# Kernel tuning notes

Measured on AMD Instinct MI355X. Metric: run time of the kernel, lower is better.

Reference implementation:

```python
import jax, jax.numpy as jnp
import numpy as np

B, L = 4, 2048
D_MODEL, D_STATE, D_CONV, N_BLOCKS = 128, 16, 8, 6
EXPAND = 2
D_INNER = EXPAND * D_MODEL          # 256
DT_RANK = (D_MODEL + 15) // 16      # 8
CONV_K = 7                          # pre_conv kernel


def setup_inputs() -> dict:
    key = jax.random.key(0)
    ks = jax.random.split(key, 10)
    f = lambda k, s: jax.random.normal(k, s, jnp.float32)
    sc = 0.02
    A_init = jnp.broadcast_to(
        jnp.log(jnp.arange(1, D_STATE + 1, dtype=jnp.float32)),
        (N_BLOCKS, D_INNER, D_STATE)) + 0.0
    return {
        "x": f(ks[0], (B, L, 1)),
        "pre_conv_w": f(ks[1], (D_MODEL, 1, CONV_K)) * sc,
        "pre_conv_b": jnp.zeros((D_MODEL,), jnp.float32),
        "ln_w": jnp.ones((N_BLOCKS, D_MODEL), jnp.float32),
        "ln_b": jnp.zeros((N_BLOCKS, D_MODEL), jnp.float32),
        "W_in": f(ks[2], (N_BLOCKS, 2 * D_INNER, D_MODEL)) * sc,
        "conv_w": f(ks[3], (N_BLOCKS, D_INNER, 1, D_CONV)) * sc,  # depthwise OIH
        "conv_b": jnp.zeros((N_BLOCKS, D_INNER), jnp.float32),
        "W_x": f(ks[4], (N_BLOCKS, DT_RANK + 2 * D_STATE, D_INNER)) * sc,
        "W_dt": f(ks[5], (N_BLOCKS, D_INNER, DT_RANK)) * sc,
        "b_dt": jnp.full((N_BLOCKS, D_INNER), -4.6, jnp.float32),  # softplus ~ 0.01
        "A_log": A_init,
        "D_skip": jnp.ones((N_BLOCKS, D_INNER), jnp.float32),
        "W_out": f(ks[6], (N_BLOCKS, D_MODEL, D_INNER)) * sc,
        "out_w": f(ks[7], (1, D_MODEL)) * sc,
        "out_b": jnp.zeros((1,), jnp.float32),
    }


def _layernorm(x, w, b, eps=1e-5):
    m = jnp.mean(x, axis=-1, keepdims=True)
    v = jnp.mean(jnp.square(x - m), axis=-1, keepdims=True)
    return (x - m) * jax.lax.rsqrt(v + eps) * w + b


def _mamba(x, W_in, cw, cb, W_x, W_dt, b_dt, A_log, D_skip, W_out):
    # x: (B, L, D_MODEL)
    xz = jnp.einsum('bld,ed->ble', x, W_in)            # (B,L,2E)
    xi, z = jnp.split(xz, 2, axis=-1)
    # depthwise causal conv over time
    xc = jax.lax.conv_general_dilated(
        xi.transpose(0, 2, 1), cw, window_strides=(1,),
        padding=[(D_CONV - 1, 0)],
        dimension_numbers=('NCH', 'OIH', 'NCH'),
        feature_group_count=D_INNER) + cb[None, :, None]
    xc = jax.nn.silu(xc).transpose(0, 2, 1)            # (B,L,E)
    dbl = jnp.einsum('ble,re->blr', xc, W_x)
    dt = dbl[..., :DT_RANK]
    Bm = dbl[..., DT_RANK:DT_RANK + D_STATE]           # (B,L,N)
    Cm = dbl[..., DT_RANK + D_STATE:]                  # (B,L,N)
    delta = jax.nn.softplus(jnp.einsum('blr,er->ble', dt, W_dt) + b_dt)
    A = -jnp.exp(A_log)                                # (E,N)

    def step(h, inp):
        d, b, c, u = inp                               # (B,E),(B,N),(B,N),(B,E)
        h = h * jnp.exp(d[..., None] * A) + (d * u)[..., None] * b[:, None, :]
        return h, jnp.einsum('ben,bn->be', h, c)

    h0 = jnp.zeros((x.shape[0], D_INNER, D_STATE), x.dtype)
    xs = (delta.transpose(1, 0, 2), Bm.transpose(1, 0, 2),
          Cm.transpose(1, 0, 2), xc.transpose(1, 0, 2))
    _, ys = jax.lax.scan(step, h0, xs)                 # ys: (L,B,E)
    y = ys.transpose(1, 0, 2) + D_skip * xc
    y = y * jax.nn.silu(z)
    return jnp.einsum('ble,de->bld', y, W_out)


def reference(x, pre_conv_w, pre_conv_b, ln_w, ln_b, W_in, conv_w, conv_b,
              W_x, W_dt, b_dt, A_log, D_skip, W_out, out_w, out_b):
    # pre_conv (1 -> d_model), SAME padding, then exact GELU
    h = jax.lax.conv_general_dilated(
        x.transpose(0, 2, 1), pre_conv_w, window_strides=(1,),
        padding=[(CONV_K // 2, CONV_K // 2)],
        dimension_numbers=('NCH', 'OIH', 'NCH')) + pre_conv_b[None, :, None]
    h = jax.nn.gelu(h, approximate=False).transpose(0, 2, 1)  # (B,L,D)

    def block(carry, p):
        lw, lb, Wi, cw, cb, Wx, Wdt, bdt, Alog, Dsk, Wo = p
        y = _mamba(_layernorm(carry, lw, lb), Wi, cw, cb, Wx, Wdt, bdt, Alog, Dsk, Wo)
        return carry + y, None                         # dropout is identity (eval)

    h, _ = jax.lax.scan(block, h, (ln_w, ln_b, W_in, conv_w, conv_b,
                                   W_x, W_dt, b_dt, A_log, D_skip, W_out))
    return (jnp.einsum('bld,od->blo', h, out_w) + out_b)[..., 0]  # (B,L)
```

## Files before the change

### kernel.cpp

```cpp
#include <hip/hip_runtime.h>
#include <hip/hip_bf16.h>
#include <hip/hip_cooperative_groups.h>
#include <math.h>

namespace cg = cooperative_groups;

#define BB 4
#define LL 2048
#define DM 128
#define DI 256
#define DS 16
#define DTR 8
#define NB 6
#define KPRE 7
#define KC 8
#define NC 128
#define CT 16
#define NCHUNK (BB*NC)
#define BL (BB*LL)
#define SU 4

typedef __attribute__((ext_vector_type(8))) short short8v;
typedef __attribute__((ext_vector_type(4))) short short4v;
typedef __attribute__((ext_vector_type(4))) float f32x4;

__device__ __forceinline__ void store_bf16x4(__hip_bfloat16* p, float a, float b, float c, float d) {
    __hip_bfloat16 t[4] = {__float2bfloat16(a), __float2bfloat16(b),
                           __float2bfloat16(c), __float2bfloat16(d)};
    *(short4v*)p = *(const short4v*)t;
}
__device__ __forceinline__ float4 load_bf16x4(const __hip_bfloat16* p) {
    short4v raw = *(const short4v*)p;
    const __hip_bfloat16* t = (const __hip_bfloat16*)&raw;
    return make_float4(__bfloat162float(t[0]), __bfloat162float(t[1]),
                       __bfloat162float(t[2]), __bfloat162float(t[3]));
}


__device__ __forceinline__ void dev_preconv(int idx,
    const float* __restrict__ x, const float* __restrict__ w, const float* __restrict__ bias,
    float* __restrict__ h, const float* __restrict__ Wi, const float* __restrict__ Wo,
    __hip_bfloat16* __restrict__ wi, __hip_bfloat16* __restrict__ wo) {
    int d = idx & (DM - 1);
    int l = (idx >> 7) & (LL - 1);
    int b = idx >> 18;
    float acc = bias[d];
#pragma unroll
    for (int k = 0; k < KPRE; ++k) {
        int pos = l + k - 3;
        float xv = (pos >= 0 && pos < LL) ? x[b * LL + pos] : 0.f;
        acc = fmaf(xv, w[d * KPRE + k], acc);
    }
    h[idx] = 0.5f * acc * (1.f + erff(acc * 0.70710678118654752f));
    if (idx < NB * 2 * DI * DM) wi[idx] = __float2bfloat16(Wi[idx]);
    if (idx < NB * DM * DI)     wo[idx] = __float2bfloat16(Wo[idx]);
}

__device__ __forceinline__ void dev_phaseA(int chunk, int tid,
    const float* __restrict__ h, const float* __restrict__ lw, const float* __restrict__ lb,
    const __hip_bfloat16* __restrict__ Wi,
    const float* __restrict__ cw, const float* __restrict__ cbs,
    const float* __restrict__ Wx, const float* __restrict__ Wdt, const float* __restrict__ bdt,
    const float* __restrict__ A_log,
    __hip_bfloat16* __restrict__ P, __hip_bfloat16* __restrict__ hend,
    __hip_bfloat16* __restrict__ z_bf,
    __hip_bfloat16* As, __hip_bfloat16 (*xi_s)[DI],
    float (*xc_s)[DI], float (*dl_s)[DI], float (*bc_s)[32]) {
    int c = chunk & (NC - 1);
    int b = chunk >> 7;
    int wave = tid >> 6, lane = tid & 63;
    for (int it = 0; it < 8; ++it) {
        int lr = wave * 8 + it;
        int tl = c * CT + lr - 16;
        int sw = (lr & 7) << 3;
        if (tl >= 0) {
            int t = b * LL + tl;
            float v0 = h[t * DM + lane];
            float v1 = h[t * DM + lane + 64];
            float s = v0 + v1;
#pragma unroll
            for (int off = 32; off; off >>= 1) s += __shfl_xor(s, off);
            float mean = s * (1.f / 128.f);
            float d0 = v0 - mean, d1 = v1 - mean;
            float q = d0 * d0 + d1 * d1;
#pragma unroll
            for (int off = 32; off; off >>= 1) q += __shfl_xor(q, off);
            float rstd = rsqrtf(q * (1.f / 128.f) + 1e-5f);
            As[lr * 128 + (lane ^ sw)]        = __float2bfloat16(d0 * rstd * lw[lane] + lb[lane]);
            As[lr * 128 + ((lane + 64) ^ sw)] = __float2bfloat16(d1 * rstd * lw[lane + 64] + lb[lane + 64]);
        } else {
            As[lr * 128 + (lane ^ sw)]        = __float2bfloat16(0.f);
            As[lr * 128 + ((lane + 64) ^ sw)] = __float2bfloat16(0.f);
        }
    }
    __syncthreads();
    {
        int r = lane & 15, kh = lane >> 4;
        short8v af[2][4];
#pragma unroll
        for (int mf = 0; mf < 2; ++mf)
#pragma unroll
            for (int k = 0; k < 4; ++k) {
                int row = mf * 16 + r;
                int cbk = k * 4 + kh;
                af[mf][k] = *(const short8v*)&As[row * 128 + ((cbk ^ (row & 7)) << 3)];
            }
        int nBase = wave * 128;
        for (int nf = 0; nf < 8; ++nf) {
            short8v bfr[4];
#pragma unroll
            for (int k = 0; k < 4; ++k)
                bfr[k] = *(const short8v*)&Wi[(size_t)(nBase + nf * 16 + r) * DM + k * 32 + kh * 8];
            if (wave < 2) {
                f32x4 acc0 = {}, acc1 = {};
#pragma unroll
                for (int k = 0; k < 4; ++k) {
                    acc0 = __builtin_amdgcn_mfma_f32_16x16x32_bf16(af[0][k], bfr[k], acc0, 0, 0, 0);
                    acc1 = __builtin_amdgcn_mfma_f32_16x16x32_bf16(af[1][k], bfr[k], acc1, 0, 0, 0);
                }
#pragma unroll
                for (int rg = 0; rg < 4; ++rg) {
                    xi_s[kh * 4 + rg][nBase + nf * 16 + r]      = __float2bfloat16(acc0[rg]);
                    xi_s[16 + kh * 4 + rg][nBase + nf * 16 + r] = __float2bfloat16(acc1[rg]);
                }
            } else {
                f32x4 acc1 = {};
#pragma unroll
                for (int k = 0; k < 4; ++k)
                    acc1 = __builtin_amdgcn_mfma_f32_16x16x32_bf16(af[1][k], bfr[k], acc1, 0, 0, 0);
#pragma unroll
                for (int rg = 0; rg < 4; ++rg)
                    z_bf[(size_t)(b * LL + c * CT + kh * 4 + rg) * DI
                         + (nBase - 256) + nf * 16 + r] = __float2bfloat16(acc1[rg]);
            }
        }
    }
    __syncthreads();
    for (int i = 0; i < 4; ++i) {
        int lt = wave * 4 + i;
        float xv[4];
        for (int j = 0; j < 4; ++j) {
            int e = lane + 64 * j;
            float4 c0 = *(const float4*)&cw[e * KC];
            float4 c1 = *(const float4*)&cw[e * KC + 4];
            float wts[8] = {c0.x, c0.y, c0.z, c0.w, c1.x, c1.y, c1.z, c1.w};
            float acc = cbs[e];
#pragma unroll
            for (int k = 0; k < KC; ++k)
                acc = fmaf(__bfloat162float(xi_s[lt + 9 + k][e]), wts[k], acc);
            xv[j] = acc / (1.f + __expf(-acc));
            xc_s[lt][e] = xv[j];
        }
        float dt8[8];
        float bcv = 0.f;
#pragma unroll
        for (int o = 0; o < 40; ++o) {
            const float* w = &Wx[o * DI];
            float s = xv[0] * w[lane];
            s = fmaf(xv[1], w[lane + 64], s);
            s = fmaf(xv[2], w[lane + 128], s);
            s = fmaf(xv[3], w[lane + 192], s);
#pragma unroll
            for (int off = 32; off; off >>= 1) s += __shfl_xor(s, off);
            if (o < 8) dt8[o] = s;
            else if (lane == o - 8) bcv = s;
        }
        if (lane < 32) bc_s[lt][lane] = bcv;
        for (int j = 0; j < 4; ++j) {
            int e = lane + 64 * j;
            float s = bdt[e];
#pragma unroll
            for (int r = 0; r < 8; ++r) s = fmaf(dt8[r], Wdt[e * 8 + r], s);
            dl_s[lt][e] = fmaxf(s, 0.f) + log1pf(__expf(-fabsf(s)));
        }
    }
    __syncthreads();
    int e = tid;
    float d16[CT], u16[CT];
#pragma unroll
    for (int l = 0; l < CT; ++l) { d16[l] = dl_s[l][e]; u16[l] = xc_s[l][e]; }
    for (int ng = 0; ng < 4; ++ng) {
        float4 al = *(const float4*)&A_log[e * DS + 4 * ng];
        float Aen[4] = {-__expf(al.x), -__expf(al.y), -__expf(al.z), -__expf(al.w)};
        float hh[4] = {}, Pl[4] = {1.f, 1.f, 1.f, 1.f};
#pragma unroll
        for (int l = 0; l < CT; ++l) {
            float du = d16[l] * u16[l];
            float4 bm = *(const float4*)&bc_s[l][4 * ng];
            float a0 = __expf(d16[l] * Aen[0]);
            float a1 = __expf(d16[l] * Aen[1]);
            float a2 = __expf(d16[l] * Aen[2]);
            float a3 = __expf(d16[l] * Aen[3]);
            hh[0] = fmaf(hh[0], a0, du * bm.x);
            hh[1] = fmaf(hh[1], a1, du * bm.y);
            hh[2] = fmaf(hh[2], a2, du * bm.z);
            hh[3] = fmaf(hh[3], a3, du * bm.w);
            Pl[0] *= a0; Pl[1] *= a1; Pl[2] *= a2; Pl[3] *= a3;
        }
        size_t oidx = (((size_t)(b * NC + c)) * DI + e) * DS + 4 * ng;
        store_bf16x4(&P[oidx], Pl[0], Pl[1], Pl[2], Pl[3]);
        store_bf16x4(&hend[oidx], hh[0], hh[1], hh[2], hh[3]);
    }
}

__device__ __forceinline__ void dev_carry(int gtid,
    const __hip_bfloat16* __restrict__ P, const __hip_bfloat16* __restrict__ hend,
    __hip_bfloat16* __restrict__ hin) {
    int n = gtid & 15;
    int e = (gtid >> 4) & 255;
    int b = gtid >> 12;
    const size_t cs = (size_t)DI * DS;
    size_t idx0 = (((size_t)(b * NC)) * DI + e) * DS + n;
    float carry = 0.f;
    for (int c0 = 0; c0 < NC; c0 += 8) {
        float p[8], he[8];
#pragma unroll
        for (int j = 0; j < 8; ++j) {
            size_t idx = idx0 + (size_t)(c0 + j) * cs;
            p[j]  = __bfloat162float(P[idx]);
            he[j] = __bfloat162float(hend[idx]);
        }
#pragma unroll
        for (int j = 0; j < 8; ++j) {
            hin[idx0 + (size_t)(c0 + j) * cs] = __float2bfloat16(carry);
            carry = fmaf(p[j], carry, he[j]);
        }
    }
}

__device__ __forceinline__ void dev_fusedB(int chunk, int tid,
    const float* __restrict__ A_log, const __hip_bfloat16* __restrict__ hin,
    const __hip_bfloat16* __restrict__ z_bf, const float* __restrict__ Dsk,
    const __hip_bfloat16* __restrict__ Wo, float* __restrict__ hout,
    const float (*xc_s)[DI], const float (*dl_s)[DI], const float (*bc_s)[32],
    __hip_bfloat16 (*y_s)[DI + 8]) {
    int c = chunk & (NC - 1);
    int b = chunk >> 7;
    int base = b * LL + c * CT;
    int e = tid;
    float d16[CT], u16[CT], yacc[CT];
    float dsk = Dsk[e];
#pragma unroll
    for (int l = 0; l < CT; ++l) {
        d16[l] = dl_s[l][e];
        u16[l] = xc_s[l][e];
        yacc[l] = dsk * u16[l];
    }
    for (int ng = 0; ng < 4; ++ng) {
        float4 al = *(const float4*)&A_log[e * DS + 4 * ng];
        float Aen[4] = {-__expf(al.x), -__expf(al.y), -__expf(al.z), -__expf(al.w)};
        float4 h4 = load_bf16x4(&hin[(((size_t)(b * NC + c)) * DI + e) * DS + 4 * ng]);
        float hh[4] = {h4.x, h4.y, h4.z, h4.w};
#pragma unroll
        for (int l = 0; l < CT; ++l) {
            float du = d16[l] * u16[l];
            float4 bm = *(const float4*)&bc_s[l][4 * ng];
            float4 cm = *(const float4*)&bc_s[l][16 + 4 * ng];
            float a0 = __expf(d16[l] * Aen[0]);
            float a1 = __expf(d16[l] * Aen[1]);
            float a2 = __expf(d16[l] * Aen[2]);
            float a3 = __expf(d16[l] * Aen[3]);
            hh[0] = fmaf(hh[0], a0, du * bm.x);
            hh[1] = fmaf(hh[1], a1, du * bm.y);
            hh[2] = fmaf(hh[2], a2, du * bm.z);
            hh[3] = fmaf(hh[3], a3, du * bm.w);
            float p = hh[0] * cm.x;
            p = fmaf(hh[1], cm.y, p);
            p = fmaf(hh[2], cm.z, p);
            p = fmaf(hh[3], cm.w, p);
            yacc[l] += p;
        }
    }
#pragma unroll
    for (int l = 0; l < CT; ++l) {
        float z = __bfloat162float(z_bf[(size_t)(base + l) * DI + e]);
        y_s[l][e] = __float2bfloat16(yacc[l] * (z / (1.f + __expf(-z))));
    }
    __syncthreads();
    int wave = tid >> 6, lane = tid & 63;
    int r  = lane & 15;
    int kh = lane >> 4;
    f32x4 acc[2] = {};
    for (int k0 = 0; k0 < DI; k0 += 32) {
        short8v af = *(const short8v*)&y_s[r][k0 + kh * 8];
        short8v bf[2];
#pragma unroll
        for (int j = 0; j < 2; ++j)
            bf[j] = *(const short8v*)&Wo[(size_t)(wave * 32 + j * 16 + r) * DI + k0 + kh * 8];
#pragma unroll
        for (int j = 0; j < 2; ++j)
            acc[j] = __builtin_amdgcn_mfma_f32_16x16x32_bf16(af, bf[j], acc[j], 0, 0, 0);
    }
    __syncthreads();
#pragma unroll
    for (int j = 0; j < 2; ++j)
#pragma unroll
        for (int rg = 0; rg < 4; ++rg) {
            size_t off = (size_t)(base + kh * 4 + rg) * DM + wave * 32 + j * 16 + r;
            hout[off] += acc[j][rg];
        }
}

__device__ __forceinline__ void dev_out(int t, int lane,
    const float* __restrict__ h, const float* __restrict__ ow, const float* __restrict__ ob,
    float* __restrict__ out) {
    float s = h[t * DM + lane] * ow[lane] + h[t * DM + lane + 64] * ow[lane + 64];
#pragma unroll
    for (int off = 32; off; off >>= 1) s += __shfl_xor(s, off);
    if (lane == 0) out[t] = s + ob[0];
}


__device__ __forceinline__ void dev_ln_gemm1(int v, int wave, int lane,
    const float* __restrict__ h, const float* __restrict__ lw, const float* __restrict__ lb,
    const __hip_bfloat16* __restrict__ W, float* __restrict__ xz,
    __hip_bfloat16* As) {
    int tileM = v >> 2, tileN = v & 3;
    int mBase = tileM * 64, nBase = tileN * 128;
    for (int it = 0; it < 16; ++it) {
        int row = wave * 16 + it;
        int t = mBase + row;
        float v0 = h[t * DM + lane];
        float v1 = h[t * DM + lane + 64];
        float s = v0 + v1;
#pragma unroll
        for (int off = 32; off; off >>= 1) s += __shfl_xor(s, off);
        float mean = s * (1.f / 128.f);
        float d0 = v0 - mean, d1 = v1 - mean;
        float q = d0 * d0 + d1 * d1;
#pragma unroll
        for (int off = 32; off; off >>= 1) q += __shfl_xor(q, off);
        float rstd = rsqrtf(q * (1.f / 128.f) + 1e-5f);
        int sw = (row & 7) << 3;
        As[row * 128 + (lane ^ sw)]        = __float2bfloat16(d0 * rstd * lw[lane] + lb[lane]);
        As[row * 128 + ((lane + 64) ^ sw)] = __float2bfloat16(d1 * rstd * lw[lane + 64] + lb[lane + 64]);
    }
    __syncthreads();
    int r  = lane & 15;
    int kh = lane >> 4;
    f32x4 acc[4][2] = {};
    for (int k0 = 0; k0 < DM; k0 += 32) {
        short8v af[4], bf[2];
#pragma unroll
        for (int i = 0; i < 4; ++i) {
            int row = i * 16 + r;
            int cbk = (k0 >> 3) + kh;
            af[i] = *(const short8v*)&As[row * 128 + ((cbk ^ (row & 7)) << 3)];
        }
#pragma unroll
        for (int j = 0; j < 2; ++j)
            bf[j] = *(const short8v*)&W[(size_t)(nBase + wave * 32 + j * 16 + r) * DM + k0 + kh * 8];
#pragma unroll
        for (int i = 0; i < 4; ++i)
#pragma unroll
            for (int j = 0; j < 2; ++j)
                acc[i][j] = __builtin_amdgcn_mfma_f32_16x16x32_bf16(af[i], bf[j], acc[i][j], 0, 0, 0);
    }
#pragma unroll
    for (int i = 0; i < 4; ++i)
#pragma unroll
        for (int j = 0; j < 2; ++j)
#pragma unroll
            for (int rg = 0; rg < 4; ++rg) {
                size_t off = (size_t)(mBase + i * 16 + kh * 4 + rg) * (2 * DI)
                           + nBase + wave * 32 + j * 16 + r;
                xz[off] = acc[i][j][rg];
            }
    __syncthreads();
}

__device__ __forceinline__ void dev_conv_wx(int t, int lane,
    const float* __restrict__ xz, const float* __restrict__ cw, const float* __restrict__ cbs,
    const float* __restrict__ Wx, const float* __restrict__ Wdt, const float* __restrict__ bdt,
    float* __restrict__ xc, float* __restrict__ BC, float* __restrict__ delta) {
    int tl = t & (LL - 1);
    int b = t >> 11;
    float xv[4];
#pragma unroll
    for (int j = 0; j < 4; ++j) {
        int e = lane + 64 * j;
        float4 cw0 = *(const float4*)&cw[e * KC];
        float4 cw1 = *(const float4*)&cw[e * KC + 4];
        float wts[8] = {cw0.x, cw0.y, cw0.z, cw0.w, cw1.x, cw1.y, cw1.z, cw1.w};
        float acc = cbs[e];
#pragma unroll
        for (int k = 0; k < KC; ++k) {
            int pos = tl + k - (KC - 1);
            float v = (pos >= 0) ? xz[((size_t)(b * LL + pos) << 9) + e] : 0.f;
            acc = fmaf(v, wts[k], acc);
        }
        xv[j] = acc / (1.f + __expf(-acc));
        xc[((size_t)t << 8) + e] = xv[j];
    }
    float dt[8];
    float bcv = 0.f;
#pragma unroll
    for (int o = 0; o < 40; ++o) {
        const float* w = &Wx[o * DI];
        float s = xv[0] * w[lane];
        s = fmaf(xv[1], w[lane + 64], s);
        s = fmaf(xv[2], w[lane + 128], s);
        s = fmaf(xv[3], w[lane + 192], s);
#pragma unroll
        for (int off = 32; off; off >>= 1) s += __shfl_xor(s, off);
        if (o < 8) dt[o] = s;
        else if (lane == o - 8) bcv = s;
    }
    if (lane < 32) BC[((size_t)t << 5) + lane] = bcv;
#pragma unroll
    for (int j = 0; j < 4; ++j) {
        int e = lane + 64 * j;
        float s = bdt[e];
#pragma unroll
        for (int r = 0; r < 8; ++r) s = fmaf(dt[r], Wdt[e * 8 + r], s);
        delta[((size_t)t << 8) + e] = fmaxf(s, 0.f) + log1pf(__expf(-fabsf(s)));
    }
}

__device__ __forceinline__ void dev_scan1(int blk, int tid,
    const float* __restrict__ delta, const float* __restrict__ xc, const float* __restrict__ BC,
    const float* __restrict__ A_log,
    __hip_bfloat16* __restrict__ P, __hip_bfloat16* __restrict__ hend) {
    int eg = blk & 3;
    int c = (blk >> 2) & (NC - 1);
    int b = blk >> 9;
    int e = eg * 64 + (tid >> 2);
    int ng = tid & 3;
    float4 al = *(const float4*)&A_log[e * DS + 4 * ng];
    float Aen[4] = {-__expf(al.x), -__expf(al.y), -__expf(al.z), -__expf(al.w)};
    float h[4] = {}, Pl[4] = {1.f, 1.f, 1.f, 1.f};
    int base = b * LL + c * CT;
    const float* dp = delta + (size_t)base * DI + e;
    const float* up = xc + (size_t)base * DI + e;
    const float* bp = BC + (size_t)base * 32 + 4 * ng;
    for (int l0 = 0; l0 < CT; l0 += SU) {
        float d[SU], u[SU];
        float4 bm[SU];
#pragma unroll
        for (int j = 0; j < SU; ++j) {
            d[j]  = dp[(l0 + j) * DI];
            u[j]  = up[(l0 + j) * DI];
            bm[j] = *(const float4*)&bp[(l0 + j) * 32];
        }
#pragma unroll
        for (int j = 0; j < SU; ++j) {
            float du = d[j] * u[j];
            float a0 = __expf(d[j] * Aen[0]);
            float a1 = __expf(d[j] * Aen[1]);
            float a2 = __expf(d[j] * Aen[2]);
            float a3 = __expf(d[j] * Aen[3]);
            h[0] = fmaf(h[0], a0, du * bm[j].x);
            h[1] = fmaf(h[1], a1, du * bm[j].y);
            h[2] = fmaf(h[2], a2, du * bm[j].z);
            h[3] = fmaf(h[3], a3, du * bm[j].w);
            Pl[0] *= a0; Pl[1] *= a1; Pl[2] *= a2; Pl[3] *= a3;
        }
    }
    size_t oidx = (((size_t)(b * NC + c)) * DI + e) * DS + 4 * ng;
    store_bf16x4(&P[oidx], Pl[0], Pl[1], Pl[2], Pl[3]);
    store_bf16x4(&hend[oidx], h[0], h[1], h[2], h[3]);
}

__device__ __forceinline__ void dev_scan3(int blk, int tid,
    const float* __restrict__ delta, const float* __restrict__ xc, const float* __restrict__ BC,
    const float* __restrict__ A_log, const __hip_bfloat16* __restrict__ hin,
    const float* __restrict__ xz,
    const float* __restrict__ Dsk, __hip_bfloat16* __restrict__ y) {
    int eg = blk & 3;
    int c = (blk >> 2) & (NC - 1);
    int b = blk >> 9;
    int e = eg * 64 + (tid >> 2);
    int ng = tid & 3;
    float4 al = *(const float4*)&A_log[e * DS + 4 * ng];
    float Aen[4] = {-__expf(al.x), -__expf(al.y), -__expf(al.z), -__expf(al.w)};
    float dsk = Dsk[e];
    float4 h4 = load_bf16x4(&hin[(((size_t)(b * NC + c)) * DI + e) * DS + 4 * ng]);
    float h[4] = {h4.x, h4.y, h4.z, h4.w};
    int base = b * LL + c * CT;
    const float* dp = delta + (size_t)base * DI + e;
    const float* up = xc + (size_t)base * DI + e;
    const float* bp = BC + (size_t)base * 32 + 4 * ng;
    const float* zp = xz + ((size_t)base << 9) + DI + e;
    __hip_bfloat16* yp = y + (size_t)base * DI + e;
    for (int l0 = 0; l0 < CT; l0 += SU) {
        float d[SU], u[SU], zv[SU];
        float4 bm[SU], cm[SU];
#pragma unroll
        for (int j = 0; j < SU; ++j) {
            d[j]  = dp[(l0 + j) * DI];
            u[j]  = up[(l0 + j) * DI];
            bm[j] = *(const float4*)&bp[(l0 + j) * 32];
            cm[j] = *(const float4*)&bp[(l0 + j) * 32 + 16];
            zv[j] = zp[(size_t)(l0 + j) << 9];
        }
#pragma unroll
        for (int j = 0; j < SU; ++j) {
            float du = d[j] * u[j];
            float a0 = __expf(d[j] * Aen[0]);
            float a1 = __expf(d[j] * Aen[1]);
            float a2 = __expf(d[j] * Aen[2]);
            float a3 = __expf(d[j] * Aen[3]);
            h[0] = fmaf(h[0], a0, du * bm[j].x);
            h[1] = fmaf(h[1], a1, du * bm[j].y);
            h[2] = fmaf(h[2], a2, du * bm[j].z);
            h[3] = fmaf(h[3], a3, du * bm[j].w);
            float yc = h[0] * cm[j].x;
            yc = fmaf(h[1], cm[j].y, yc);
            yc = fmaf(h[2], cm[j].z, yc);
            yc = fmaf(h[3], cm[j].w, yc);
            yc += __shfl_xor(yc, 1);
            yc += __shfl_xor(yc, 2);
            if (ng == 0) {
                float z = zv[j];
                float val = (yc + dsk * u[j]) * (z / (1.f + __expf(-z)));
                yp[(l0 + j) * DI] = __float2bfloat16(val);
            }
        }
    }
}

__device__ __forceinline__ void dev_gemm2(int v, int wave, int lane,
    const __hip_bfloat16* __restrict__ A, const __hip_bfloat16* __restrict__ W,
    float* __restrict__ C) {
    int mBase = v * 16;
    int r  = lane & 15;
    int kh = lane >> 4;
    f32x4 acc[2] = {};
    for (int k0 = 0; k0 < DI; k0 += 32) {
        short8v af = *(const short8v*)&A[(size_t)(mBase + r) * DI + k0 + kh * 8];
        short8v bf[2];
#pragma unroll
        for (int j = 0; j < 2; ++j)
            bf[j] = *(const short8v*)&W[(size_t)(wave * 32 + j * 16 + r) * DI + k0 + kh * 8];
#pragma unroll
        for (int j = 0; j < 2; ++j)
            acc[j] = __builtin_amdgcn_mfma_f32_16x16x32_bf16(af, bf[j], acc[j], 0, 0, 0);
    }
#pragma unroll
    for (int j = 0; j < 2; ++j)
#pragma unroll
        for (int rg = 0; rg < 4; ++rg) {
            size_t off = (size_t)(mBase + kh * 4 + rg) * DM + wave * 32 + j * 16 + r;
            C[off] += acc[j][rg];
        }
}


struct MegaArgs {
    const float *x, *pcw, *pcb, *ln_w, *ln_b, *conv_w, *conv_b;
    const float *W_x, *W_dt, *b_dt, *A_log, *D_skip, *W_in, *W_out, *out_w, *out_b;
    float *h, *out;
    __hip_bfloat16 *P, *hend, *hin, *z_bf, *wi_bf, *wo_bf;
};

__global__ __launch_bounds__(256, 2) void k_mega(MegaArgs a) {
    __shared__ union {
        struct {
            __hip_bfloat16 As[32 * 128];
            __hip_bfloat16 xi[32][DI];
        } pa;
        __hip_bfloat16 y_s[CT][DI + 8];
    } u;
    __shared__ float xc_s[CT][DI];
    __shared__ float dl_s[CT][DI];
    __shared__ float bc_s[CT][32];
    cg::grid_group g = cg::this_grid();
    int bid = blockIdx.x, tid = threadIdx.x;
    int nb = gridDim.x;
    int wave = tid >> 6, lane = tid & 63;

    for (int v = bid; v < (BB * LL * DM) / 256; v += nb)
        dev_preconv(v * 256 + tid, a.x, a.pcw, a.pcb, a.h, a.W_in, a.W_out, a.wi_bf, a.wo_bf);
    g.sync();

    for (int blk = 0; blk < NB; ++blk) {
        dev_phaseA(bid, tid, a.h, a.ln_w + blk * DM, a.ln_b + blk * DM,
                   a.wi_bf + (size_t)blk * 2 * DI * DM,
                   a.conv_w + (size_t)blk * DI * KC, a.conv_b + blk * DI,
                   a.W_x + (size_t)blk * 40 * DI, a.W_dt + (size_t)blk * DI * DTR,
                   a.b_dt + blk * DI, a.A_log + (size_t)blk * DI * DS,
                   a.P, a.hend, a.z_bf, u.pa.As, u.pa.xi, xc_s, dl_s, bc_s);
        g.sync();
        for (int v = bid; v < (BB * DI * DS) / 256; v += nb)
            dev_carry(v * 256 + tid, a.P, a.hend, a.hin);
        g.sync();
        dev_fusedB(bid, tid, a.A_log + (size_t)blk * DI * DS, a.hin, a.z_bf,
                   a.D_skip + blk * DI, a.wo_bf + (size_t)blk * DM * DI, a.h,
                   xc_s, dl_s, bc_s, u.y_s);
        g.sync();
    }

    for (int v = bid; v < BL / 4; v += nb)
        dev_out(v * 4 + wave, lane, a.h, a.out_w, a.out_b, a.out);
}


__global__ void w_preconv(const float* x, const float* w, const float* bias, float* h,
                          const float* Wi, const float* Wo,
                          __hip_bfloat16* wi, __hip_bfloat16* wo) {
    dev_preconv(blockIdx.x * 256 + threadIdx.x, x, w, bias, h, Wi, Wo, wi, wo);
}
__global__ __launch_bounds__(256) void w_ln_gemm1(const float* h, const float* lw, const float* lb,
                                                  const __hip_bfloat16* W, float* xz) {
    __shared__ __hip_bfloat16 As[64 * 128];
    dev_ln_gemm1(blockIdx.x, threadIdx.x >> 6, threadIdx.x & 63, h, lw, lb, W, xz, As);
}
__global__ __launch_bounds__(256) void w_conv_wx(const float* xz, const float* cw, const float* cbs,
                                                 const float* Wx, const float* Wdt, const float* bdt,
                                                 float* xc, float* BC, float* delta) {
    dev_conv_wx(blockIdx.x * 4 + (threadIdx.x >> 6), threadIdx.x & 63,
                xz, cw, cbs, Wx, Wdt, bdt, xc, BC, delta);
}
__global__ __launch_bounds__(256) void w_scan1(const float* delta, const float* xc, const float* BC,
                                               const float* A_log,
                                               __hip_bfloat16* P, __hip_bfloat16* hend) {
    dev_scan1(blockIdx.x, threadIdx.x, delta, xc, BC, A_log, P, hend);
}
__global__ void w_carry(const __hip_bfloat16* P, const __hip_bfloat16* hend, __hip_bfloat16* hin) {
    dev_carry(blockIdx.x * 256 + threadIdx.x, P, hend, hin);
}
__global__ __launch_bounds__(256) void w_scan3(const float* delta, const float* xc, const float* BC,
                                               const float* A_log, const __hip_bfloat16* hin,
                                               const float* xz,
                                               const float* Dsk, __hip_bfloat16* y) {
    dev_scan3(blockIdx.x, threadIdx.x, delta, xc, BC, A_log, hin, xz, Dsk, y);
}
__global__ __launch_bounds__(256) void w_gemm2(const __hip_bfloat16* A, const __hip_bfloat16* W,
                                               float* C) {
    dev_gemm2(blockIdx.x, threadIdx.x >> 6, threadIdx.x & 63, A, W, C);
}
__global__ void w_out(const float* h, const float* ow, const float* ob, float* out) {
    dev_out(blockIdx.x * 4 + (threadIdx.x >> 6), threadIdx.x & 63, h, ow, ob, out);
}

extern "C" void kernel_launch(void* const* d_in, const int* in_sizes, int n_in,
                              void* d_out, int out_size, void* d_ws, size_t ws_size,
                              hipStream_t stream) {
    (void)in_sizes; (void)n_in; (void)out_size; (void)ws_size;
    const float* x      = (const float*)d_in[0];
    const float* pcw    = (const float*)d_in[1];
    const float* pcb    = (const float*)d_in[2];
    const float* ln_w   = (const float*)d_in[3];
    const float* ln_b   = (const float*)d_in[4];
    const float* W_in   = (const float*)d_in[5];
    const float* conv_w = (const float*)d_in[6];
    const float* conv_b = (const float*)d_in[7];
    const float* W_x    = (const float*)d_in[8];
    const float* W_dt   = (const float*)d_in[9];
    const float* b_dt   = (const float*)d_in[10];
    const float* A_log  = (const float*)d_in[11];
    const float* D_skip = (const float*)d_in[12];
    const float* W_out  = (const float*)d_in[13];
    const float* out_w  = (const float*)d_in[14];
    const float* out_b  = (const float*)d_in[15];

    const size_t SCAN_N = (size_t)BB * NC * DI * DS;
    float* ws    = (float*)d_ws;
    float* h     = ws;
    float* xz    = h     + (size_t)BL * DM;
    float* xc    = xz    + (size_t)BL * 2 * DI;
    float* BC    = xc    + (size_t)BL * DI;
    float* delta = BC    + (size_t)BL * 2 * DS;
    __hip_bfloat16* P    = (__hip_bfloat16*)(delta + (size_t)BL * DI);
    __hip_bfloat16* hend = P + SCAN_N;
    __hip_bfloat16* hin  = hend + SCAN_N;
    __hip_bfloat16* y_bf  = hin + SCAN_N;
    __hip_bfloat16* z_bf  = y_bf + (size_t)BL * DI;
    __hip_bfloat16* wi_bf = z_bf + (size_t)BL * DI;
    __hip_bfloat16* wo_bf = wi_bf + (size_t)NB * 2 * DI * DM;

    int dev = 0;
    (void)hipGetDevice(&dev);
    int coopAttr = 0;
    (void)hipDeviceGetAttribute(&coopAttr, hipDeviceAttributeCooperativeLaunch, dev);
    int numCU = 0;
    (void)hipDeviceGetAttribute(&numCU, hipDeviceAttributeMultiprocessorCount, dev);
    int maxBpCU = 0;
    (void)hipOccupancyMaxActiveBlocksPerMultiprocessor(&maxBpCU, k_mega, 256, 0);
    int grid = maxBpCU * numCU;
    if (grid > NCHUNK) grid = NCHUNK;

    bool launched = false;
    if (coopAttr && grid == NCHUNK) {
        MegaArgs ma = {x, pcw, pcb, ln_w, ln_b, conv_w, conv_b,
                       W_x, W_dt, b_dt, A_log, D_skip, W_in, W_out, out_w, out_b,
                       h, (float*)d_out,
                       P, hend, hin, z_bf, wi_bf, wo_bf};
        void* kp[] = {&ma};
        hipError_t e = hipLaunchCooperativeKernel((void*)k_mega, dim3(grid), dim3(256), kp, 0, stream);
        launched = (e == hipSuccess);
        if (!launched) (void)hipGetLastError();
    }

    if (!launched) {
        w_preconv<<<(BB * LL * DM) / 256, 256, 0, stream>>>(x, pcw, pcb, h, W_in, W_out, wi_bf, wo_bf);
        for (int blk = 0; blk < NB; ++blk) {
            w_ln_gemm1<<<512, 256, 0, stream>>>(
                h, ln_w + blk * DM, ln_b + blk * DM, wi_bf + (size_t)blk * 2 * DI * DM, xz);
            w_conv_wx<<<BL / 4, 256, 0, stream>>>(
                xz, conv_w + (size_t)blk * DI * KC, conv_b + blk * DI,
                W_x + (size_t)blk * 40 * DI, W_dt + (size_t)blk * DI * DTR,
                b_dt + blk * DI, xc, BC, delta);
            w_scan1<<<BB * NC * 4, 256, 0, stream>>>(
                delta, xc, BC, A_log + (size_t)blk * DI * DS, P, hend);
            w_carry<<<(BB * DI * DS) / 256, 256, 0, stream>>>(P, hend, hin);
            w_scan3<<<BB * NC * 4, 256, 0, stream>>>(
                delta, xc, BC, A_log + (size_t)blk * DI * DS, hin, xz, D_skip + blk * DI, y_bf);
            w_gemm2<<<BL / 16, 256, 0, stream>>>(y_bf, wo_bf + (size_t)blk * DM * DI, h);
        }
        w_out<<<BL / 4, 256, 0, stream>>>(h, out_w, out_b, (float*)d_out);
    }
}
```

Baseline: 562.0 us.

## Replace grid-wide carry pass with decoupled look-back chunk scan and LDS-resident z

Removes the two grid syncs and the separate carry phase in each block. Each chunk now publishes its aggregate (P, hend) and inclusive state through per-chunk flags, then walks back over its predecessors until it finds an inclusive prefix, in the style of a decoupled look-back scan. The z half of the input projection and the chunk's incoming state now stay in shared memory instead of making a round trip through global buffers. This adds spin-waiting on flags with serial dependencies across chunks, and raises LDS use, which may reduce occupancy.

```diff
diff --git a/kernel.cpp b/kernel.cpp
--- a/kernel.cpp
+++ b/kernel.cpp
@@ -35,6 +35,21 @@
     return make_float4(__bfloat162float(t[0]), __bfloat162float(t[1]),
                        __bfloat162float(t[2]), __bfloat162float(t[3]));
 }
+__device__ __forceinline__ void load_bf16x16(const __hip_bfloat16* p, float* o) {
+    short8v a = *(const short8v*)p;
+    short8v b = *(const short8v*)(p + 8);
+    const __hip_bfloat16* ta = (const __hip_bfloat16*)&a;
+    const __hip_bfloat16* tb = (const __hip_bfloat16*)&b;
+#pragma unroll
+    for (int i = 0; i < 8; ++i) { o[i] = __bfloat162float(ta[i]); o[8 + i] = __bfloat162float(tb[i]); }
+}
+__device__ __forceinline__ void store_bf16x16(__hip_bfloat16* p, const float* v) {
+    __hip_bfloat16 t[16];
+#pragma unroll
+    for (int i = 0; i < 16; ++i) t[i] = __float2bfloat16(v[i]);
+    *(short8v*)p = *(const short8v*)t;
+    *(short8v*)(p + 8) = *(const short8v*)(t + 8);
+}
 
 
 __device__ __forceinline__ void dev_preconv(int idx,
@@ -56,16 +71,17 @@
     if (idx < NB * DM * DI)     wo[idx] = __float2bfloat16(Wo[idx]);
 }
 
-__device__ __forceinline__ void dev_phaseA(int chunk, int tid,
+__device__ __forceinline__ void dev_phaseA(int chunk, int tid, int epoch,
     const float* __restrict__ h, const float* __restrict__ lw, const float* __restrict__ lb,
     const __hip_bfloat16* __restrict__ Wi,
     const float* __restrict__ cw, const float* __restrict__ cbs,
     const float* __restrict__ Wx, const float* __restrict__ Wdt, const float* __restrict__ bdt,
     const float* __restrict__ A_log,
-    __hip_bfloat16* __restrict__ P, __hip_bfloat16* __restrict__ hend,
-    __hip_bfloat16* __restrict__ z_bf,
+    __hip_bfloat16* __restrict__ Pst, __hip_bfloat16* __restrict__ hend,
+    __hip_bfloat16* __restrict__ hincl, int* __restrict__ flags,
     __hip_bfloat16* As, __hip_bfloat16 (*xi_s)[DI],
-    float (*xc_s)[DI], float (*dl_s)[DI], float (*bc_s)[32]) {
+    float (*xc_s)[DI], float (*dl_s)[DI], float (*bc_s)[32],
+    __hip_bfloat16 (*z_s)[DI], __hip_bfloat16 (*hin_s)[DS]) {
     int c = chunk & (NC - 1);
     int b = chunk >> 7;
     int wave = tid >> 6, lane = tid & 63;
@@ -130,8 +146,7 @@
                     acc1 = __builtin_amdgcn_mfma_f32_16x16x32_bf16(af[1][k], bfr[k], acc1, 0, 0, 0);
 #pragma unroll
                 for (int rg = 0; rg < 4; ++rg)
-                    z_bf[(size_t)(b * LL + c * CT + kh * 4 + rg) * DI
-                         + (nBase - 256) + nf * 16 + r] = __float2bfloat16(acc1[rg]);
+                    z_s[kh * 4 + rg][(nBase - 256) + nf * 16 + r] = __float2bfloat16(acc1[rg]);
             }
         }
     }
@@ -176,63 +191,101 @@
     }
     __syncthreads();
     int e = tid;
-    float d16[CT], u16[CT];
-#pragma unroll
-    for (int l = 0; l < CT; ++l) { d16[l] = dl_s[l][e]; u16[l] = xc_s[l][e]; }
-    for (int ng = 0; ng < 4; ++ng) {
-        float4 al = *(const float4*)&A_log[e * DS + 4 * ng];
-        float Aen[4] = {-__expf(al.x), -__expf(al.y), -__expf(al.z), -__expf(al.w)};
-        float hh[4] = {}, Pl[4] = {1.f, 1.f, 1.f, 1.f};
-#pragma unroll
-        for (int l = 0; l < CT; ++l) {
-            float du = d16[l] * u16[l];
-            float4 bm = *(const float4*)&bc_s[l][4 * ng];
-            float a0 = __expf(d16[l] * Aen[0]);
-            float a1 = __expf(d16[l] * Aen[1]);
-            float a2 = __expf(d16[l] * Aen[2]);
-            float a3 = __expf(d16[l] * Aen[3]);
-            hh[0] = fmaf(hh[0], a0, du * bm.x);
-            hh[1] = fmaf(hh[1], a1, du * bm.y);
-            hh[2] = fmaf(hh[2], a2, du * bm.z);
-            hh[3] = fmaf(hh[3], a3, du * bm.w);
-            Pl[0] *= a0; Pl[1] *= a1; Pl[2] *= a2; Pl[3] *= a3;
-        }
-        size_t oidx = (((size_t)(b * NC + c)) * DI + e) * DS + 4 * ng;
-        store_bf16x4(&P[oidx], Pl[0], Pl[1], Pl[2], Pl[3]);
-        store_bf16x4(&hend[oidx], hh[0], hh[1], hh[2], hh[3]);
-    }
-}
-
-__device__ __forceinline__ void dev_carry(int gtid,
-    const __hip_bfloat16* __restrict__ P, const __hip_bfloat16* __restrict__ hend,
-    __hip_bfloat16* __restrict__ hin) {
-    int n = gtid & 15;
-    int e = (gtid >> 4) & 255;
-    int b = gtid >> 12;
-    const size_t cs = (size_t)DI * DS;
-    size_t idx0 = (((size_t)(b * NC)) * DI + e) * DS + n;
-    float carry = 0.f;
-    for (int c0 = 0; c0 < NC; c0 += 8) {
-        float p[8], he[8];
-#pragma unroll
-        for (int j = 0; j < 8; ++j) {
-            size_t idx = idx0 + (size_t)(c0 + j) * cs;
-            p[j]  = __bfloat162float(P[idx]);
-            he[j] = __bfloat162float(hend[idx]);
-        }
-#pragma unroll
-        for (int j = 0; j < 8; ++j) {
-            hin[idx0 + (size_t)(c0 + j) * cs] = __float2bfloat16(carry);
-            carry = fmaf(p[j], carry, he[j]);
-        }
-    }
+    {
+        float d16[CT], u16[CT];
+#pragma unroll
+        for (int l = 0; l < CT; ++l) { d16[l] = dl_s[l][e]; u16[l] = xc_s[l][e]; }
+        for (int ng = 0; ng < 4; ++ng) {
+            float4 al = *(const float4*)&A_log[e * DS + 4 * ng];
+            float Aen[4] = {-__expf(al.x), -__expf(al.y), -__expf(al.z), -__expf(al.w)};
+            float hh[4] = {}, Pl[4] = {1.f, 1.f, 1.f, 1.f};
+#pragma unroll
+            for (int l = 0; l < CT; ++l) {
+                float du = d16[l] * u16[l];
+                float4 bm = *(const float4*)&bc_s[l][4 * ng];
+                float a0 = __expf(d16[l] * Aen[0]);
+                float a1 = __expf(d16[l] * Aen[1]);
+                float a2 = __expf(d16[l] * Aen[2]);
+                float a3 = __expf(d16[l] * Aen[3]);
+                hh[0] = fmaf(hh[0], a0, du * bm.x);
+                hh[1] = fmaf(hh[1], a1, du * bm.y);
+                hh[2] = fmaf(hh[2], a2, du * bm.z);
+                hh[3] = fmaf(hh[3], a3, du * bm.w);
+                Pl[0] *= a0; Pl[1] *= a1; Pl[2] *= a2; Pl[3] *= a3;
+            }
+            size_t oidx = (((size_t)(b * NC + c)) * DI + e) * DS + 4 * ng;
+            store_bf16x4(&Pst[oidx], Pl[0], Pl[1], Pl[2], Pl[3]);
+            store_bf16x4(&hend[oidx], hh[0], hh[1], hh[2], hh[3]);
+        }
+    }
+    __threadfence();
+    __syncthreads();
+    if (tid == 0)
+        __hip_atomic_store(&flags[b * NC + c], 2 * epoch,
+                           __ATOMIC_RELEASE, __HIP_MEMORY_SCOPE_AGENT);
+    float hacc[16], Pacc[16];
+#pragma unroll
+    for (int n = 0; n < 16; ++n) { hacc[n] = 0.f; Pacc[n] = 1.f; }
+    int j = c - 1;
+    while (j >= 0) {
+        int j2 = (j >= 1) ? j - 1 : j;
+        int f1, f0;
+        do {
+            f1 = __hip_atomic_load(&flags[b * NC + j],  __ATOMIC_ACQUIRE, __HIP_MEMORY_SCOPE_AGENT);
+            f0 = __hip_atomic_load(&flags[b * NC + j2], __ATOMIC_ACQUIRE, __HIP_MEMORY_SCOPE_AGENT);
+            if (f1 < 2 * epoch || f0 < 2 * epoch) __builtin_amdgcn_s_sleep(2);
+        } while (f1 < 2 * epoch || f0 < 2 * epoch);
+        size_t bj = (((size_t)(b * NC + j)) * DI + e) * DS;
+        if (f1 > 2 * epoch) {
+            float hi[16]; load_bf16x16(&hincl[bj], hi);
+#pragma unroll
+            for (int n = 0; n < 16; ++n) hacc[n] = fmaf(Pacc[n], hi[n], hacc[n]);
+            break;
+        }
+        float pj[16], he[16];
+        load_bf16x16(&Pst[bj], pj);
+        load_bf16x16(&hend[bj], he);
+#pragma unroll
+        for (int n = 0; n < 16; ++n) { hacc[n] = fmaf(Pacc[n], he[n], hacc[n]); Pacc[n] *= pj[n]; }
+        if (j == 0) break;
+        size_t bj0 = (((size_t)(b * NC + j - 1)) * DI + e) * DS;
+        if (f0 > 2 * epoch) {
+            float hi[16]; load_bf16x16(&hincl[bj0], hi);
+#pragma unroll
+            for (int n = 0; n < 16; ++n) hacc[n] = fmaf(Pacc[n], hi[n], hacc[n]);
+            break;
+        }
+        float pj0[16], he0[16];
+        load_bf16x16(&Pst[bj0], pj0);
+        load_bf16x16(&hend[bj0], he0);
+#pragma unroll
+        for (int n = 0; n < 16; ++n) { hacc[n] = fmaf(Pacc[n], he0[n], hacc[n]); Pacc[n] *= pj0[n]; }
+        j -= 2;
+    }
+    {
+        size_t bcx = (((size_t)(b * NC + c)) * DI + e) * DS;
+        float pc[16], hc[16];
+        load_bf16x16(&Pst[bcx], pc);
+        load_bf16x16(&hend[bcx], hc);
+#pragma unroll
+        for (int n = 0; n < 16; ++n) {
+            hin_s[e][n] = __float2bfloat16(hacc[n]);
+            hc[n] = fmaf(pc[n], hacc[n], hc[n]);
+        }
+        store_bf16x16(&hincl[bcx], hc);
+    }
+    __threadfence();
+    __syncthreads();
+    if (tid == 0)
+        __hip_atomic_store(&flags[b * NC + c], 2 * epoch + 1,
+                           __ATOMIC_RELEASE, __HIP_MEMORY_SCOPE_AGENT);
 }
 
 __device__ __forceinline__ void dev_fusedB(int chunk, int tid,
-    const float* __restrict__ A_log, const __hip_bfloat16* __restrict__ hin,
-    const __hip_bfloat16* __restrict__ z_bf, const float* __restrict__ Dsk,
+    const float* __restrict__ A_log, const float* __restrict__ Dsk,
     const __hip_bfloat16* __restrict__ Wo, float* __restrict__ hout,
     const float (*xc_s)[DI], const float (*dl_s)[DI], const float (*bc_s)[32],
+    const __hip_bfloat16 (*z_s)[DI], const __hip_bfloat16 (*hin_s)[DS],
     __hip_bfloat16 (*y_s)[DI + 8]) {
     int c = chunk & (NC - 1);
     int b = chunk >> 7;
@@ -249,8 +302,10 @@
     for (int ng = 0; ng < 4; ++ng) {
         float4 al = *(const float4*)&A_log[e * DS + 4 * ng];
         float Aen[4] = {-__expf(al.x), -__expf(al.y), -__expf(al.z), -__expf(al.w)};
-        float4 h4 = load_bf16x4(&hin[(((size_t)(b * NC + c)) * DI + e) * DS + 4 * ng]);
-        float hh[4] = {h4.x, h4.y, h4.z, h4.w};
+        float hh[4] = {__bfloat162float(hin_s[e][4 * ng]),
+                       __bfloat162float(hin_s[e][4 * ng + 1]),
+                       __bfloat162float(hin_s[e][4 * ng + 2]),
+                       __bfloat162float(hin_s[e][4 * ng + 3])};
 #pragma unroll
         for (int l = 0; l < CT; ++l) {
             float du = d16[l] * u16[l];
@@ -273,7 +328,7 @@
     }
 #pragma unroll
     for (int l = 0; l < CT; ++l) {
-        float z = __bfloat162float(z_bf[(size_t)(base + l) * DI + e]);
+        float z = __bfloat162float(z_s[l][e]);
         y_s[l][e] = __float2bfloat16(yacc[l] * (z / (1.f + __expf(-z))));
     }
     __syncthreads();
@@ -285,19 +340,19 @@
         short8v af = *(const short8v*)&y_s[r][k0 + kh * 8];
         short8v bf[2];
 #pragma unroll
-        for (int j = 0; j < 2; ++j)
-            bf[j] = *(const short8v*)&Wo[(size_t)(wave * 32 + j * 16 + r) * DI + k0 + kh * 8];
-#pragma unroll
-        for (int j = 0; j < 2; ++j)
-            acc[j] = __builtin_amdgcn_mfma_f32_16x16x32_bf16(af, bf[j], acc[j], 0, 0, 0);
-    }
-    __syncthreads();
-#pragma unroll
-    for (int j = 0; j < 2; ++j)
+        for (int jj = 0; jj < 2; ++jj)
+            bf[jj] = *(const short8v*)&Wo[(size_t)(wave * 32 + jj * 16 + r) * DI + k0 + kh * 8];
+#pragma unroll
+        for (int jj = 0; jj < 2; ++jj)
+            acc[jj] = __builtin_amdgcn_mfma_f32_16x16x32_bf16(af, bf[jj], acc[jj], 0, 0, 0);
+    }
+    __syncthreads();
+#pragma unroll
+    for (int jj = 0; jj < 2; ++jj)
 #pragma unroll
         for (int rg = 0; rg < 4; ++rg) {
-            size_t off = (size_t)(base + kh * 4 + rg) * DM + wave * 32 + j * 16 + r;
-            hout[off] += acc[j][rg];
+            size_t off = (size_t)(base + kh * 4 + rg) * DM + wave * 32 + jj * 16 + r;
+            hout[off] += acc[jj][rg];
         }
 }
 
@@ -459,6 +514,31 @@
     size_t oidx = (((size_t)(b * NC + c)) * DI + e) * DS + 4 * ng;
     store_bf16x4(&P[oidx], Pl[0], Pl[1], Pl[2], Pl[3]);
     store_bf16x4(&hend[oidx], h[0], h[1], h[2], h[3]);
+}
+
+__device__ __forceinline__ void dev_carry(int gtid,
+    const __hip_bfloat16* __restrict__ P, const __hip_bfloat16* __restrict__ hend,
+    __hip_bfloat16* __restrict__ hin) {
+    int n = gtid & 15;
+    int e = (gtid >> 4) & 255;
+    int b = gtid >> 12;
+    const size_t cs = (size_t)DI * DS;
+    size_t idx0 = (((size_t)(b * NC)) * DI + e) * DS + n;
+    float carry = 0.f;
+    for (int c0 = 0; c0 < NC; c0 += 8) {
+        float p[8], he[8];
+#pragma unroll
+        for (int j = 0; j < 8; ++j) {
+            size_t idx = idx0 + (size_t)(c0 + j) * cs;
+            p[j]  = __bfloat162float(P[idx]);
+            he[j] = __bfloat162float(hend[idx]);
+        }
+#pragma unroll
+        for (int j = 0; j < 8; ++j) {
+            hin[idx0 + (size_t)(c0 + j) * cs] = __float2bfloat16(carry);
+            carry = fmaf(p[j], carry, he[j]);
+        }
+    }
 }
 
 __device__ __forceinline__ void dev_scan3(int blk, int tid,
@@ -550,7 +630,8 @@
     const float *x, *pcw, *pcb, *ln_w, *ln_b, *conv_w, *conv_b;
     const float *W_x, *W_dt, *b_dt, *A_log, *D_skip, *W_in, *W_out, *out_w, *out_b;
     float *h, *out;
-    __hip_bfloat16 *P, *hend, *hin, *z_bf, *wi_bf, *wo_bf;
+    __hip_bfloat16 *P, *hend, *hincl, *wi_bf, *wo_bf;
+    int *flags;
 };
 
 __global__ __launch_bounds__(256, 2) void k_mega(MegaArgs a) {
@@ -564,29 +645,29 @@
     __shared__ float xc_s[CT][DI];
     __shared__ float dl_s[CT][DI];
     __shared__ float bc_s[CT][32];
+    __shared__ __hip_bfloat16 z_s[CT][DI];
+    __shared__ __hip_bfloat16 hin_s[DI][DS];
     cg::grid_group g = cg::this_grid();
     int bid = blockIdx.x, tid = threadIdx.x;
     int nb = gridDim.x;
     int wave = tid >> 6, lane = tid & 63;
 
+    for (int v = bid * 256 + tid; v < NCHUNK; v += nb * 256) a.flags[v] = 0;
     for (int v = bid; v < (BB * LL * DM) / 256; v += nb)
         dev_preconv(v * 256 + tid, a.x, a.pcw, a.pcb, a.h, a.W_in, a.W_out, a.wi_bf, a.wo_bf);
     g.sync();
 
     for (int blk = 0; blk < NB; ++blk) {
-        dev_phaseA(bid, tid, a.h, a.ln_w + blk * DM, a.ln_b + blk * DM,
+        dev_phaseA(bid, tid, blk + 1, a.h, a.ln_w + blk * DM, a.ln_b + blk * DM,
                    a.wi_bf + (size_t)blk * 2 * DI * DM,
                    a.conv_w + (size_t)blk * DI * KC, a.conv_b + blk * DI,
                    a.W_x + (size_t)blk * 40 * DI, a.W_dt + (size_t)blk * DI * DTR,
                    a.b_dt + blk * DI, a.A_log + (size_t)blk * DI * DS,
-                   a.P, a.hend, a.z_bf, u.pa.As, u.pa.xi, xc_s, dl_s, bc_s);
-        g.sync();
-        for (int v = bid; v < (BB * DI * DS) / 256; v += nb)
-            dev_carry(v * 256 + tid, a.P, a.hend, a.hin);
-        g.sync();
-        dev_fusedB(bid, tid, a.A_log + (size_t)blk * DI * DS, a.hin, a.z_bf,
+                   a.P, a.hend, a.hincl, a.flags,
+                   u.pa.As, u.pa.xi, xc_s, dl_s, bc_s, z_s, hin_s);
+        dev_fusedB(bid, tid, a.A_log + (size_t)blk * DI * DS,
                    a.D_skip + blk * DI, a.wo_bf + (size_t)blk * DM * DI, a.h,
-                   xc_s, dl_s, bc_s, u.y_s);
+                   xc_s, dl_s, bc_s, z_s, hin_s, u.y_s);
         g.sync();
     }
 
@@ -661,13 +742,14 @@
     float* xc    = xz    + (size_t)BL * 2 * DI;
     float* BC    = xc    + (size_t)BL * DI;
     float* delta = BC    + (size_t)BL * 2 * DS;
-    __hip_bfloat16* P    = (__hip_bfloat16*)(delta + (size_t)BL * DI);
-    __hip_bfloat16* hend = P + SCAN_N;
-    __hip_bfloat16* hin  = hend + SCAN_N;
-    __hip_bfloat16* y_bf  = hin + SCAN_N;
-    __hip_bfloat16* z_bf  = y_bf + (size_t)BL * DI;
-    __hip_bfloat16* wi_bf = z_bf + (size_t)BL * DI;
+    __hip_bfloat16* P     = (__hip_bfloat16*)(delta + (size_t)BL * DI);
+    __hip_bfloat16* hend  = P + SCAN_N;
+    __hip_bfloat16* hin   = hend + SCAN_N;
+    __hip_bfloat16* hincl = hin + SCAN_N;
+    __hip_bfloat16* y_bf  = hincl + SCAN_N;
+    __hip_bfloat16* wi_bf = y_bf + (size_t)BL * DI;
     __hip_bfloat16* wo_bf = wi_bf + (size_t)NB * 2 * DI * DM;
+    int* flags = (int*)(wo_bf + (size_t)NB * DM * DI);
 
     int dev = 0;
     (void)hipGetDevice(&dev);
@@ -685,7 +767,7 @@
         MegaArgs ma = {x, pcw, pcb, ln_w, ln_b, conv_w, conv_b,
                        W_x, W_dt, b_dt, A_log, D_skip, W_in, W_out, out_w, out_b,
                        h, (float*)d_out,
-                       P, hend, hin, z_bf, wi_bf, wo_bf};
+                       P, hend, hincl, wi_bf, wo_bf, flags};
         void* kp[] = {&ma};
         hipError_t e = hipLaunchCooperativeKernel((void*)k_mega, dim3(grid), dim3(256), kp, 0, stream);
         launched = (e == hipSuccess);
```

New measurement: 562.5 us. No clear change (+0.1%).
